# Optimization experiments

Measured on AMD Instinct MI355X. Metric: run time of the kernel, lower is better.

The kernel has to match this reference:

```python
import jax, jax.numpy as jnp
import numpy as np

NEG_SLOPE = 0.2   # PyG GATConv default negative_slope
LN_EPS = 1e-5

B, N, D, HID, HEADS = 4, 10000, 128, 256, 2
F_HEAD = HID // HEADS  # 128
E_RAND = 160000


def setup_inputs() -> dict:
    key = jax.random.key(0)
    ks = jax.random.split(key, 12)
    src = jax.random.randint(ks[0], (E_RAND,), 0, N, dtype=jnp.int32)
    dst = jax.random.randint(ks[1], (E_RAND,), 0, N, dtype=jnp.int32)
    loops = jnp.arange(N, dtype=jnp.int32)  # PyG GATConv adds self-loops
    edge_index = jnp.stack([jnp.concatenate([src, loops]),
                            jnp.concatenate([dst, loops])])  # [2, 170000]
    feature = jax.random.normal(ks[2], (B, N, D), jnp.float32)

    def w(k, shape):
        return jax.random.normal(k, shape, jnp.float32) * 0.05

    return {
        "feature": feature,
        "edge_index": edge_index,
        # layer 1: in D=128 -> heads*F_HEAD = 256
        "W1": w(ks[3], (D, HEADS * F_HEAD)),
        "a_src1": w(ks[4], (HEADS, F_HEAD)),
        "a_dst1": w(ks[5], (HEADS, F_HEAD)),
        "b1": jnp.zeros((HEADS * F_HEAD,), jnp.float32),
        "g1": jnp.ones((HID,), jnp.float32),
        "be1": jnp.zeros((HID,), jnp.float32),
        # layer 2: in 256 -> 256
        "W2": w(ks[6], (HID, HEADS * F_HEAD)),
        "a_src2": w(ks[7], (HEADS, F_HEAD)),
        "a_dst2": w(ks[8], (HEADS, F_HEAD)),
        "b2": jnp.zeros((HEADS * F_HEAD,), jnp.float32),
        "g2": jnp.ones((HID,), jnp.float32),
        "be2": jnp.zeros((HID,), jnp.float32),
    }


def _layer_norm(x, g, b):
    mu = jnp.mean(x, axis=-1, keepdims=True)
    var = jnp.mean(jnp.square(x - mu), axis=-1, keepdims=True)
    return (x - mu) * jax.lax.rsqrt(var + LN_EPS) * g + b


def _gat_conv(x, src, dst, W, a_src, a_dst, b):
    """PyG-style GATConv (concat=True), single graph. x: [N, Din]."""
    n = x.shape[0]
    h = (x @ W).reshape(n, HEADS, F_HEAD)              # [N,H,F]
    al_s = jnp.sum(h * a_src, axis=-1)                  # [N,H]
    al_d = jnp.sum(h * a_dst, axis=-1)                  # [N,H]
    e = jax.nn.leaky_relu(al_s[src] + al_d[dst], NEG_SLOPE)  # [E,H]
    # segment softmax over destination node (self-loops guarantee nonempty)
    m = jax.ops.segment_max(e, dst, num_segments=n)     # [N,H]
    ex = jnp.exp(e - m[dst])
    denom = jax.ops.segment_sum(ex, dst, num_segments=n)
    alpha = ex / (denom[dst] + 1e-16)                   # [E,H]
    msg = h[src] * alpha[..., None]                     # [E,H,F]
    out = jax.ops.segment_sum(msg, dst, num_segments=n) # [N,H,F]
    return out.reshape(n, HEADS * F_HEAD) + b


def reference(feature, edge_index, W1, a_src1, a_dst1, b1, g1, be1,
              W2, a_src2, a_dst2, b2, g2, be2):
    src, dst = edge_index[0], edge_index[1]

    def per_graph(x):
        h = _gat_conv(x, src, dst, W1, a_src1, a_dst1, b1)
        h = jax.nn.relu(_layer_norm(h, g1, be1))  # dropout off (eval)
        h = _gat_conv(h, src, dst, W2, a_src2, a_dst2, b2)
        h = jax.nn.relu(_layer_norm(h, g2, be2))
        return h

    return jax.vmap(per_graph)(feature)  # [B, N, HID]
```

## Files before the change

### kernel.cpp

```cpp
#include <hip/hip_runtime.h>
#include <hip/hip_bf16.h>

#define NN   10000
#define BB   4
#define DD   128
#define HIDD 256
#define NEG  0.2f

using bf16 = __hip_bfloat16;
typedef __bf16 bf16x8 __attribute__((ext_vector_type(8)));
typedef float  f32x4  __attribute__((ext_vector_type(4)));

__device__ __forceinline__ float lrelu(float x) { return x > 0.f ? x : NEG * x; }

__device__ __forceinline__ unsigned pack2(float a, float b) {
    unsigned lo = __bfloat16_as_ushort(__float2bfloat16(a));
    unsigned hi = __bfloat16_as_ushort(__float2bfloat16(b));
    return lo | (hi << 16);
}

__global__ void convert_kernel(const float* __restrict__ x, bf16* __restrict__ y, int n) {
    int i = blockIdx.x * 256 + threadIdx.x;
    if (i < n) y[i] = __float2bfloat16(x[i]);
}

__global__ void prep_kernel(int* counts,
                            const float* __restrict__ W1, bf16* __restrict__ Wt1,
                            const float* __restrict__ W2, bf16* __restrict__ Wt2) {
    int idx = blockIdx.x * 256 + threadIdx.x;
    if (idx < NN) { counts[idx] = 0; return; }
    idx -= NN;
    if (idx < DD * HIDD) {
        int k = idx / HIDD, n = idx % HIDD;
        Wt1[(size_t)n * DD + k] = __float2bfloat16(W1[idx]);
        return;
    }
    idx -= DD * HIDD;
    if (idx < HIDD * HIDD) {
        int k = idx / HIDD, n = idx % HIDD;
        Wt2[(size_t)n * HIDD + k] = __float2bfloat16(W2[idx]);
    }
}

__global__ void hist_kernel(const int* __restrict__ dstv, int* counts, int E) {
    int e = blockIdx.x * 256 + threadIdx.x;
    if (e < E) atomicAdd(&counts[dstv[e]], 1);
}

__global__ __launch_bounds__(1024) void scan_kernel(const int* __restrict__ counts,
                                                    int* row_start, int* cursor) {
    __shared__ int part[1024];
    int t = threadIdx.x;
    const int CH = (NN + 1023) / 1024;
    int base = t * CH;
    int s = 0;
    for (int j = 0; j < CH; j++) { int idx = base + j; if (idx < NN) s += counts[idx]; }
    part[t] = s;
    __syncthreads();
    for (int off = 1; off < 1024; off <<= 1) {
        int v = (t >= off) ? part[t - off] : 0;
        __syncthreads();
        part[t] += v;
        __syncthreads();
    }
    int excl = (t == 0) ? 0 : part[t - 1];
    for (int j = 0; j < CH; j++) {
        int idx = base + j;
        if (idx < NN) { row_start[idx] = excl; cursor[idx] = excl; excl += counts[idx]; }
    }
    if (t == 1023) row_start[NN] = part[1023];
}

__global__ void scatter_kernel(const int* __restrict__ srcv, const int* __restrict__ dstv,
                               int* cursor, int* csr_src, int E) {
    int e = blockIdx.x * 256 + threadIdx.x;
    if (e < E) {
        int d = dstv[e];
        int p = atomicAdd(&cursor[d], 1);
        csr_src[p] = srcv[e];
    }
}

template <int K>
__global__ __launch_bounds__(256) void gemm_kernel(const bf16* __restrict__ A,
                                                   const bf16* __restrict__ Wt,
                                                   const float* __restrict__ a_src,
                                                   const float* __restrict__ a_dst,
                                                   bf16* __restrict__ H,
                                                   float* __restrict__ als,
                                                   float* __restrict__ ald) {
    constexpr int NF = K / 32;
    __shared__ bf16 Bs[8 * NF * 512];

    int b     = blockIdx.x;
    int g     = b & 3;
    int r     = b >> 2;
    int head  = r & 1;
    int split = r >> 1;
    int wave  = threadIdx.x >> 6, lane = threadIdx.x & 63;
    int lm    = lane & 15, lq = lane >> 4;

    const bf16* Wh = Wt + (size_t)head * 128 * K;

#pragma unroll
    for (int jj = 0; jj < 2 * NF; jj++) {
        int j  = wave * 2 * NF + jj;
        int fi = j / NF, ks = j % NF;
        const bf16* src = Wh + (size_t)(fi * 16 + lm) * K + ks * 32 + lq * 8;
        __builtin_amdgcn_global_load_lds(
            (const __attribute__((address_space(1))) void*)src,
            (__attribute__((address_space(3))) void*)(Bs + j * 512),
            16, 0, 0);
    }
    __syncthreads();

    float4 asv[8], adv[8];
#pragma unroll
    for (int fi = 0; fi < 8; fi++) {
        asv[fi] = *(const float4*)(a_src + head * 128 + fi * 16 + lq * 4);
        adv[fi] = *(const float4*)(a_dst + head * 128 + fi * 16 + lq * 4);
    }

    const int NT = (NN + 127) / 128;
    for (int tt = split; tt < NT; tt += 64) {
        int m0 = tt * 128 + wave * 32;
        int rA = min(m0 + lm, NN - 1);
        int rB = min(m0 + 16 + lm, NN - 1);
        const bf16* Ar0 = A + ((size_t)g * NN + rA) * K + lq * 8;
        const bf16* Ar1 = A + ((size_t)g * NN + rB) * K + lq * 8;

        bf16x8 a0[NF], a1[NF];
#pragma unroll
        for (int ks = 0; ks < NF; ks++) {
            a0[ks] = *(const bf16x8*)(Ar0 + ks * 32);
            a1[ks] = *(const bf16x8*)(Ar1 + ks * 32);
        }

        f32x4 acc[2][8];
#pragma unroll
        for (int rb = 0; rb < 2; rb++)
#pragma unroll
            for (int i = 0; i < 8; i++) acc[rb][i] = (f32x4){0.f, 0.f, 0.f, 0.f};

#pragma unroll
        for (int ks = 0; ks < NF; ks++) {
#pragma unroll
            for (int fi = 0; fi < 8; fi++) {
                bf16x8 bv = *(const bf16x8*)(Bs + ((size_t)(fi * NF + ks) * 64 + lane) * 8);
                acc[0][fi] = __builtin_amdgcn_mfma_f32_16x16x32_bf16(bv, a0[ks], acc[0][fi], 0, 0, 0);
                acc[1][fi] = __builtin_amdgcn_mfma_f32_16x16x32_bf16(bv, a1[ks], acc[1][fi], 0, 0, 0);
            }
        }

#pragma unroll
        for (int rb = 0; rb < 2; rb++) {
            int nd = m0 + rb * 16 + lm;
            float ps = 0.f, pd = 0.f;
            bool ok = nd < NN;
            size_t hb = ((size_t)g * NN + (ok ? nd : 0)) * HIDD + head * 128 + lq * 4;
#pragma unroll
            for (int fi = 0; fi < 8; fi++) {
                f32x4 v = acc[rb][fi];
                ps += v[0] * asv[fi].x + v[1] * asv[fi].y + v[2] * asv[fi].z + v[3] * asv[fi].w;
                pd += v[0] * adv[fi].x + v[1] * adv[fi].y + v[2] * adv[fi].z + v[3] * adv[fi].w;
                if (ok) {
                    uint2 pk = {pack2(v[0], v[1]), pack2(v[2], v[3])};
                    *(uint2*)(H + hb + fi * 16) = pk;
                }
            }
            ps += __shfl_xor(ps, 16); ps += __shfl_xor(ps, 32);
            pd += __shfl_xor(pd, 16); pd += __shfl_xor(pd, 32);
            if (lq == 0 && ok) {
                als[((size_t)g * NN + nd) * 2 + head] = ps;
                ald[((size_t)g * NN + nd) * 2 + head] = pd;
            }
        }
    }
}

template <typename OT>
__global__ __launch_bounds__(256) void node_kernel(const int* __restrict__ row_start,
                                                   const int* __restrict__ csr_src,
                                                   const float2* __restrict__ als2,
                                                   const float2* __restrict__ ald2,
                                                   const bf16* __restrict__ H,
                                                   const float* __restrict__ bias,
                                                   const float* __restrict__ gam,
                                                   const float* __restrict__ bet,
                                                   OT* __restrict__ out) {
    int b = blockIdx.x;
    int g = b & 3;
    int wave = threadIdx.x >> 6, lane = threadIdx.x & 63;
    int n = (b >> 2) * 4 + wave;
    if (n >= NN) return;
    int start = row_start[n];
    int deg   = row_start[n + 1] - start;

    int grp = lane >> 5, lch = lane & 31;
    int hd_g = lch >> 4;
    const float* alsf = (const float*)(als2 + (size_t)g * NN);
    float2 ad = ald2[(size_t)g * NN + n];
    float adh = hd_g ? ad.y : ad.x;
    const int* Sr = csr_src + start;
    const bf16* Hg = H + (size_t)g * NN * HIDD;

    float acc[8] = {0.f, 0.f, 0.f, 0.f, 0.f, 0.f, 0.f, 0.f};
    float dsum = 0.f;

#define EDGE_FMA(ss, qq)                                                \
    {                                                                   \
        float wv = __expf(lrelu(alsf[(size_t)(ss) * 2 + hd_g] + adh));  \
        dsum += wv;                                                     \
        acc[0] = fmaf(wv, __uint_as_float(qq.x << 16), acc[0]);         \
        acc[1] = fmaf(wv, __uint_as_float(qq.x & 0xffff0000u), acc[1]); \
        acc[2] = fmaf(wv, __uint_as_float(qq.y << 16), acc[2]);         \
        acc[3] = fmaf(wv, __uint_as_float(qq.y & 0xffff0000u), acc[3]); \
        acc[4] = fmaf(wv, __uint_as_float(qq.z << 16), acc[4]);         \
        acc[5] = fmaf(wv, __uint_as_float(qq.z & 0xffff0000u), acc[5]); \
        acc[6] = fmaf(wv, __uint_as_float(qq.w << 16), acc[6]);         \
        acc[7] = fmaf(wv, __uint_as_float(qq.w & 0xffff0000u), acc[7]); \
    }

    int i = grp;
    for (; i + 6 < deg; i += 8) {
        int s0 = Sr[i], s1 = Sr[i + 2], s2 = Sr[i + 4], s3 = Sr[i + 6];
        uint4 q0 = *(const uint4*)(Hg + (size_t)s0 * HIDD + lch * 8);
        uint4 q1 = *(const uint4*)(Hg + (size_t)s1 * HIDD + lch * 8);
        uint4 q2 = *(const uint4*)(Hg + (size_t)s2 * HIDD + lch * 8);
        uint4 q3 = *(const uint4*)(Hg + (size_t)s3 * HIDD + lch * 8);
        EDGE_FMA(s0, q0)
        EDGE_FMA(s1, q1)
        EDGE_FMA(s2, q2)
        EDGE_FMA(s3, q3)
    }
    for (; i < deg; i += 2) {
        int s0 = Sr[i];
        uint4 q0 = *(const uint4*)(Hg + (size_t)s0 * HIDD + lch * 8);
        EDGE_FMA(s0, q0)
    }
#undef EDGE_FMA

#pragma unroll
    for (int j = 0; j < 8; j++) acc[j] += __shfl_xor(acc[j], 32);
    dsum += __shfl_xor(dsum, 32);
    float rdh = 1.f / dsum;

    float4 bi0 = *(const float4*)(bias + lch * 8);
    float4 bi1 = *(const float4*)(bias + lch * 8 + 4);
    float v[8];
    v[0] = fmaf(acc[0], rdh, bi0.x); v[1] = fmaf(acc[1], rdh, bi0.y);
    v[2] = fmaf(acc[2], rdh, bi0.z); v[3] = fmaf(acc[3], rdh, bi0.w);
    v[4] = fmaf(acc[4], rdh, bi1.x); v[5] = fmaf(acc[5], rdh, bi1.y);
    v[6] = fmaf(acc[6], rdh, bi1.z); v[7] = fmaf(acc[7], rdh, bi1.w);

    float s1 = 0.f, s2 = 0.f;
#pragma unroll
    for (int j = 0; j < 8; j++) { s1 += v[j]; s2 += v[j] * v[j]; }
#pragma unroll
    for (int off = 16; off; off >>= 1) {
        s1 += __shfl_xor(s1, off);
        s2 += __shfl_xor(s2, off);
    }
    float mu  = s1 * (1.f / HIDD);
    float var = s2 * (1.f / HIDD) - mu * mu;
    float rs  = rsqrtf(var + 1e-5f);

    float4 ga0 = *(const float4*)(gam + lch * 8);
    float4 ga1 = *(const float4*)(gam + lch * 8 + 4);
    float4 be0 = *(const float4*)(bet + lch * 8);
    float4 be1 = *(const float4*)(bet + lch * 8 + 4);
    float gaf[8] = {ga0.x, ga0.y, ga0.z, ga0.w, ga1.x, ga1.y, ga1.z, ga1.w};
    float bef[8] = {be0.x, be0.y, be0.z, be0.w, be1.x, be1.y, be1.z, be1.w};

    float o[8];
#pragma unroll
    for (int j = 0; j < 8; j++)
        o[j] = fmaxf((v[j] - mu) * rs * gaf[j] + bef[j], 0.f);

    if (grp == 0) {
        size_t base = ((size_t)g * NN + n) * HIDD + lch * 8;
        if constexpr (sizeof(OT) == 2) {
            uint4 pk;
            pk.x = pack2(o[0], o[1]); pk.y = pack2(o[2], o[3]);
            pk.z = pack2(o[4], o[5]); pk.w = pack2(o[6], o[7]);
            *(uint4*)((bf16*)out + base) = pk;
        } else {
            *(float4*)((float*)out + base)     = make_float4(o[0], o[1], o[2], o[3]);
            *(float4*)((float*)out + base + 4) = make_float4(o[4], o[5], o[6], o[7]);
        }
    }
}

extern "C" void kernel_launch(void* const* d_in, const int* in_sizes, int n_in,
                              void* d_out, int out_size, void* d_ws, size_t ws_size,
                              hipStream_t stream) {
    const float* feature = (const float*)d_in[0];
    const int*   ei      = (const int*)d_in[1];
    const float* W1      = (const float*)d_in[2];
    const float* a_src1  = (const float*)d_in[3];
    const float* a_dst1  = (const float*)d_in[4];
    const float* b1      = (const float*)d_in[5];
    const float* g1      = (const float*)d_in[6];
    const float* be1     = (const float*)d_in[7];
    const float* W2      = (const float*)d_in[8];
    const float* a_src2  = (const float*)d_in[9];
    const float* a_dst2  = (const float*)d_in[10];
    const float* b2      = (const float*)d_in[11];
    const float* g2      = (const float*)d_in[12];
    const float* be2     = (const float*)d_in[13];
    float* out = (float*)d_out;

    const int E = in_sizes[1] / 2;
    const int* srcv = ei;
    const int* dstv = ei + E;

    char* w = (char*)d_ws;
    auto alloc = [&](size_t bytes) -> char* {
        char* p = w;
        w += (bytes + 255) & ~(size_t)255;
        return p;
    };
    int*    counts    = (int*)alloc(sizeof(int) * NN);
    int*    row_start = (int*)alloc(sizeof(int) * (NN + 1));
    int*    cursor    = (int*)alloc(sizeof(int) * NN);
    int*    csr_src   = (int*)alloc(sizeof(int) * E);
    float*  als       = (float*)alloc(sizeof(float) * (size_t)BB * NN * 2);
    float*  ald       = (float*)alloc(sizeof(float) * (size_t)BB * NN * 2);
    bf16*   featbf    = (bf16*)alloc(sizeof(bf16) * (size_t)BB * NN * DD);
    bf16*   h         = (bf16*)alloc(sizeof(bf16) * (size_t)BB * NN * HIDD);
    bf16*   x2        = (bf16*)alloc(sizeof(bf16) * (size_t)BB * NN * HIDD);
    bf16*   Wt1       = (bf16*)alloc(sizeof(bf16) * DD * HIDD);
    bf16*   Wt2       = (bf16*)alloc(sizeof(bf16) * HIDD * HIDD);

    int nblk = ((NN + 3) / 4) * 4;
    int gblk = 4 * 2 * 64;

    {
        int ptot = NN + DD * HIDD + HIDD * HIDD;
        prep_kernel<<<(ptot + 255) / 256, 256, 0, stream>>>(counts, W1, Wt1, W2, Wt2);
        int nf = BB * NN * DD;
        convert_kernel<<<(nf + 255) / 256, 256, 0, stream>>>(feature, featbf, nf);
    }
    hist_kernel<<<(E + 255) / 256, 256, 0, stream>>>(dstv, counts, E);
    scan_kernel<<<1, 1024, 0, stream>>>(counts, row_start, cursor);
    scatter_kernel<<<(E + 255) / 256, 256, 0, stream>>>(srcv, dstv, cursor, csr_src, E);

    gemm_kernel<DD><<<gblk, 256, 0, stream>>>(featbf, Wt1, a_src1, a_dst1, h, als, ald);
    node_kernel<bf16><<<nblk, 256, 0, stream>>>(row_start, csr_src, (const float2*)als, (const float2*)ald,
                                                h, b1, g1, be1, x2);

    gemm_kernel<HIDD><<<gblk, 256, 0, stream>>>(x2, Wt2, a_src2, a_dst2, h, als, ald);
    node_kernel<float><<<nblk, 256, 0, stream>>>(row_start, csr_src, (const float2*)als, (const float2*)ald,
                                                 h, b2, g2, be2, out);
}
```

Measured before the change: 264.1 us.

## Use one 256-row tile per 512-thread GEMM block and deepen edge unroll

Result: slower. 285.4 us (+8.1%).

```diff
diff --git a/kernel.cpp b/kernel.cpp
--- a/kernel.cpp
+++ b/kernel.cpp
@@ -82,7 +82,7 @@
 }
 
 template <int K>
-__global__ __launch_bounds__(256) void gemm_kernel(const bf16* __restrict__ A,
+__global__ __launch_bounds__(512) void gemm_kernel(const bf16* __restrict__ A,
                                                    const bf16* __restrict__ Wt,
                                                    const float* __restrict__ a_src,
                                                    const float* __restrict__ a_dst,
@@ -96,20 +96,18 @@
     int g     = b & 3;
     int r     = b >> 2;
     int head  = r & 1;
-    int split = r >> 1;
+    int tile  = r >> 1;
     int wave  = threadIdx.x >> 6, lane = threadIdx.x & 63;
     int lm    = lane & 15, lq = lane >> 4;
 
     const bf16* Wh = Wt + (size_t)head * 128 * K;
 
 #pragma unroll
-    for (int jj = 0; jj < 2 * NF; jj++) {
-        int j  = wave * 2 * NF + jj;
-        int fi = j / NF, ks = j % NF;
-        const bf16* src = Wh + (size_t)(fi * 16 + lm) * K + ks * 32 + lq * 8;
+    for (int ks = 0; ks < NF; ks++) {
+        const bf16* src = Wh + (size_t)(wave * 16 + lm) * K + ks * 32 + lq * 8;
         __builtin_amdgcn_global_load_lds(
             (const __attribute__((address_space(1))) void*)src,
-            (__attribute__((address_space(3))) void*)(Bs + j * 512),
+            (__attribute__((address_space(3))) void*)(Bs + (wave * NF + ks) * 512),
             16, 0, 0);
     }
     __syncthreads();
@@ -121,59 +119,51 @@
         adv[fi] = *(const float4*)(a_dst + head * 128 + fi * 16 + lq * 4);
     }
 
-    const int NT = (NN + 127) / 128;
-    for (int tt = split; tt < NT; tt += 64) {
-        int m0 = tt * 128 + wave * 32;
-        int rA = min(m0 + lm, NN - 1);
-        int rB = min(m0 + 16 + lm, NN - 1);
-        const bf16* Ar0 = A + ((size_t)g * NN + rA) * K + lq * 8;
-        const bf16* Ar1 = A + ((size_t)g * NN + rB) * K + lq * 8;
-
-        bf16x8 a0[NF], a1[NF];
-#pragma unroll
-        for (int ks = 0; ks < NF; ks++) {
-            a0[ks] = *(const bf16x8*)(Ar0 + ks * 32);
-            a1[ks] = *(const bf16x8*)(Ar1 + ks * 32);
+    int m0 = tile * 256 + wave * 32;
+    int rA = min(m0 + lm, NN - 1);
+    int rB = min(m0 + 16 + lm, NN - 1);
+    const bf16* Ar0 = A + ((size_t)g * NN + rA) * K + lq * 8;
+    const bf16* Ar1 = A + ((size_t)g * NN + rB) * K + lq * 8;
+
+    f32x4 acc[2][8];
+#pragma unroll
+    for (int rb = 0; rb < 2; rb++)
+#pragma unroll
+        for (int i = 0; i < 8; i++) acc[rb][i] = (f32x4){0.f, 0.f, 0.f, 0.f};
+
+#pragma unroll
+    for (int ks = 0; ks < NF; ks++) {
+        bf16x8 a0 = *(const bf16x8*)(Ar0 + ks * 32);
+        bf16x8 a1 = *(const bf16x8*)(Ar1 + ks * 32);
+#pragma unroll
+        for (int fi = 0; fi < 8; fi++) {
+            bf16x8 bv = *(const bf16x8*)(Bs + ((size_t)(fi * NF + ks) * 64 + lane) * 8);
+            acc[0][fi] = __builtin_amdgcn_mfma_f32_16x16x32_bf16(bv, a0, acc[0][fi], 0, 0, 0);
+            acc[1][fi] = __builtin_amdgcn_mfma_f32_16x16x32_bf16(bv, a1, acc[1][fi], 0, 0, 0);
         }
-
-        f32x4 acc[2][8];
-#pragma unroll
-        for (int rb = 0; rb < 2; rb++)
-#pragma unroll
-            for (int i = 0; i < 8; i++) acc[rb][i] = (f32x4){0.f, 0.f, 0.f, 0.f};
-
-#pragma unroll
-        for (int ks = 0; ks < NF; ks++) {
-#pragma unroll
-            for (int fi = 0; fi < 8; fi++) {
-                bf16x8 bv = *(const bf16x8*)(Bs + ((size_t)(fi * NF + ks) * 64 + lane) * 8);
-                acc[0][fi] = __builtin_amdgcn_mfma_f32_16x16x32_bf16(bv, a0[ks], acc[0][fi], 0, 0, 0);
-                acc[1][fi] = __builtin_amdgcn_mfma_f32_16x16x32_bf16(bv, a1[ks], acc[1][fi], 0, 0, 0);
+    }
+
+#pragma unroll
+    for (int rb = 0; rb < 2; rb++) {
+        int nd = m0 + rb * 16 + lm;
+        float ps = 0.f, pd = 0.f;
+        bool ok = nd < NN;
+        size_t hb = ((size_t)g * NN + (ok ? nd : 0)) * HIDD + head * 128 + lq * 4;
+#pragma unroll
+        for (int fi = 0; fi < 8; fi++) {
+            f32x4 v = acc[rb][fi];
+            ps += v[0] * asv[fi].x + v[1] * asv[fi].y + v[2] * asv[fi].z + v[3] * asv[fi].w;
+            pd += v[0] * adv[fi].x + v[1] * adv[fi].y + v[2] * adv[fi].z + v[3] * adv[fi].w;
+            if (ok) {
+                uint2 pk = {pack2(v[0], v[1]), pack2(v[2], v[3])};
+                *(uint2*)(H + hb + fi * 16) = pk;
             }
         }
-
-#pragma unroll
-        for (int rb = 0; rb < 2; rb++) {
-            int nd = m0 + rb * 16 + lm;
-            float ps = 0.f, pd = 0.f;
-            bool ok = nd < NN;
-            size_t hb = ((size_t)g * NN + (ok ? nd : 0)) * HIDD + head * 128 + lq * 4;
-#pragma unroll
-            for (int fi = 0; fi < 8; fi++) {
-                f32x4 v = acc[rb][fi];
-                ps += v[0] * asv[fi].x + v[1] * asv[fi].y + v[2] * asv[fi].z + v[3] * asv[fi].w;
-                pd += v[0] * adv[fi].x + v[1] * adv[fi].y + v[2] * adv[fi].z + v[3] * adv[fi].w;
-                if (ok) {
-                    uint2 pk = {pack2(v[0], v[1]), pack2(v[2], v[3])};
-                    *(uint2*)(H + hb + fi * 16) = pk;
-                }
-            }
-            ps += __shfl_xor(ps, 16); ps += __shfl_xor(ps, 32);
-            pd += __shfl_xor(pd, 16); pd += __shfl_xor(pd, 32);
-            if (lq == 0 && ok) {
-                als[((size_t)g * NN + nd) * 2 + head] = ps;
-                ald[((size_t)g * NN + nd) * 2 + head] = pd;
-            }
+        ps += __shfl_xor(ps, 16); ps += __shfl_xor(ps, 32);
+        pd += __shfl_xor(pd, 16); pd += __shfl_xor(pd, 32);
+        if (lq == 0 && ok) {
+            als[((size_t)g * NN + nd) * 2 + head] = ps;
+            ald[((size_t)g * NN + nd) * 2 + head] = pd;
         }
     }
 }
@@ -222,6 +212,26 @@
     }
 
     int i = grp;
+    for (; i + 14 < deg; i += 16) {
+        int s0 = Sr[i],      s1 = Sr[i + 2],  s2 = Sr[i + 4],  s3 = Sr[i + 6];
+        int s4 = Sr[i + 8],  s5 = Sr[i + 10], s6 = Sr[i + 12], s7 = Sr[i + 14];
+        uint4 q0 = *(const uint4*)(Hg + (size_t)s0 * HIDD + lch * 8);
+        uint4 q1 = *(const uint4*)(Hg + (size_t)s1 * HIDD + lch * 8);
+        uint4 q2 = *(const uint4*)(Hg + (size_t)s2 * HIDD + lch * 8);
+        uint4 q3 = *(const uint4*)(Hg + (size_t)s3 * HIDD + lch * 8);
+        uint4 q4 = *(const uint4*)(Hg + (size_t)s4 * HIDD + lch * 8);
+        uint4 q5 = *(const uint4*)(Hg + (size_t)s5 * HIDD + lch * 8);
+        uint4 q6 = *(const uint4*)(Hg + (size_t)s6 * HIDD + lch * 8);
+        uint4 q7 = *(const uint4*)(Hg + (size_t)s7 * HIDD + lch * 8);
+        EDGE_FMA(s0, q0)
+        EDGE_FMA(s1, q1)
+        EDGE_FMA(s2, q2)
+        EDGE_FMA(s3, q3)
+        EDGE_FMA(s4, q4)
+        EDGE_FMA(s5, q5)
+        EDGE_FMA(s6, q6)
+        EDGE_FMA(s7, q7)
+    }
     for (; i + 6 < deg; i += 8) {
         int s0 = Sr[i], s1 = Sr[i + 2], s2 = Sr[i + 4], s3 = Sr[i + 6];
         uint4 q0 = *(const uint4*)(Hg + (size_t)s0 * HIDD + lch * 8);
@@ -333,7 +343,7 @@
     bf16*   Wt2       = (bf16*)alloc(sizeof(bf16) * HIDD * HIDD);
 
     int nblk = ((NN + 3) / 4) * 4;
-    int gblk = 4 * 2 * 64;
+    int gblk = 4 * 2 * ((NN + 255) / 256);
 
     {
         int ptot = NN + DD * HIDD + HIDD * HIDD;
@@ -345,11 +355,11 @@
     scan_kernel<<<1, 1024, 0, stream>>>(counts, row_start, cursor);
     scatter_kernel<<<(E + 255) / 256, 256, 0, stream>>>(srcv, dstv, cursor, csr_src, E);
 
-    gemm_kernel<DD><<<gblk, 256, 0, stream>>>(featbf, Wt1, a_src1, a_dst1, h, als, ald);
+    gemm_kernel<DD><<<gblk, 512, 0, stream>>>(featbf, Wt1, a_src1, a_dst1, h, als, ald);
     node_kernel<bf16><<<nblk, 256, 0, stream>>>(row_start, csr_src, (const float2*)als, (const float2*)ald,
                                                 h, b1, g1, be1, x2);
 
-    gemm_kernel<HIDD><<<gblk, 256, 0, stream>>>(x2, Wt2, a_src2, a_dst2, h, als, ald);
+    gemm_kernel<HIDD><<<gblk, 512, 0, stream>>>(x2, Wt2, a_src2, a_dst2, h, als, ald);
     node_kernel<float><<<nblk, 256, 0, stream>>>(row_start, csr_src, (const float2*)als, (const float2*)ald,
                                                  h, b2, g2, be2, out);
 }
```

## Restructure GEMM to one tile per block with K-chunked LDS and fuse feature convert

Applied to the files above, without the earlier changes.

Measured after the change: 252.1 us. 1.05x faster.

```diff
diff --git a/kernel.cpp b/kernel.cpp
--- a/kernel.cpp
+++ b/kernel.cpp
@@ -19,15 +19,19 @@
     return lo | (hi << 16);
 }
 
-__global__ void convert_kernel(const float* __restrict__ x, bf16* __restrict__ y, int n) {
-    int i = blockIdx.x * 256 + threadIdx.x;
-    if (i < n) y[i] = __float2bfloat16(x[i]);
-}
-
-__global__ void prep_kernel(int* counts,
+#define NF4 (BB * NN * DD / 4)
+__global__ void prep_kernel(const float* __restrict__ feat, bf16* __restrict__ featbf,
+                            int* counts,
                             const float* __restrict__ W1, bf16* __restrict__ Wt1,
                             const float* __restrict__ W2, bf16* __restrict__ Wt2) {
     int idx = blockIdx.x * 256 + threadIdx.x;
+    if (idx < NF4) {
+        float4 v = *(const float4*)(feat + (size_t)idx * 4);
+        uint2 pk = {pack2(v.x, v.y), pack2(v.z, v.w)};
+        *(uint2*)(featbf + (size_t)idx * 4) = pk;
+        return;
+    }
+    idx -= NF4;
     if (idx < NN) { counts[idx] = 0; return; }
     idx -= NN;
     if (idx < DD * HIDD) {
@@ -89,30 +93,59 @@
                                                    bf16* __restrict__ H,
                                                    float* __restrict__ als,
                                                    float* __restrict__ ald) {
-    constexpr int NF = K / 32;
-    __shared__ bf16 Bs[8 * NF * 512];
-
-    int b     = blockIdx.x;
-    int g     = b & 3;
-    int r     = b >> 2;
-    int head  = r & 1;
-    int split = r >> 1;
-    int wave  = threadIdx.x >> 6, lane = threadIdx.x & 63;
-    int lm    = lane & 15, lq = lane >> 4;
-
-    const bf16* Wh = Wt + (size_t)head * 128 * K;
-
-#pragma unroll
-    for (int jj = 0; jj < 2 * NF; jj++) {
-        int j  = wave * 2 * NF + jj;
-        int fi = j / NF, ks = j % NF;
-        const bf16* src = Wh + (size_t)(fi * 16 + lm) * K + ks * 32 + lq * 8;
-        __builtin_amdgcn_global_load_lds(
-            (const __attribute__((address_space(1))) void*)src,
-            (__attribute__((address_space(3))) void*)(Bs + j * 512),
-            16, 0, 0);
-    }
-    __syncthreads();
+    __shared__ bf16 Bs[128 * 128];
+
+    int b    = blockIdx.x;
+    int g    = b & 3;
+    int r    = b >> 2;
+    int head = r & 1;
+    int wave = threadIdx.x >> 6;
+    int m0   = (r >> 1) * 128 + wave * 32;
+    int lane = threadIdx.x & 63;
+    int lm   = lane & 15, lq = lane >> 4;
+
+    int rowA = min(m0 + lm, NN - 1);
+    int rowB = min(m0 + 16 + lm, NN - 1);
+    const bf16* Ar0 = A + ((size_t)g * NN + rowA) * K + lq * 8;
+    const bf16* Ar1 = A + ((size_t)g * NN + rowB) * K + lq * 8;
+    const bf16* Wh  = Wt + (size_t)head * 128 * K;
+
+    f32x4 acc[2][8];
+#pragma unroll
+    for (int rb = 0; rb < 2; rb++)
+#pragma unroll
+        for (int i = 0; i < 8; i++) acc[rb][i] = (f32x4){0.f, 0.f, 0.f, 0.f};
+
+    for (int kb = 0; kb < K; kb += 128) {
+        if (kb) __syncthreads();
+#pragma unroll
+        for (int jj = 0; jj < 8; jj++) {
+            int j  = wave * 8 + jj;
+            int fi = j >> 2, ks = j & 3;
+            const bf16* src = Wh + (size_t)(fi * 16 + lm) * K + kb + ks * 32 + lq * 8;
+            __builtin_amdgcn_global_load_lds(
+                (const __attribute__((address_space(1))) void*)src,
+                (__attribute__((address_space(3))) void*)(Bs + j * 512),
+                16, 0, 0);
+        }
+        __syncthreads();
+
+        bf16x8 a0[4], a1[4];
+#pragma unroll
+        for (int ks = 0; ks < 4; ks++) {
+            a0[ks] = *(const bf16x8*)(Ar0 + kb + ks * 32);
+            a1[ks] = *(const bf16x8*)(Ar1 + kb + ks * 32);
+        }
+#pragma unroll
+        for (int ks = 0; ks < 4; ks++) {
+#pragma unroll
+            for (int fi = 0; fi < 8; fi++) {
+                bf16x8 bv = *(const bf16x8*)(Bs + ((fi * 4 + ks) * 64 + lane) * 8);
+                acc[0][fi] = __builtin_amdgcn_mfma_f32_16x16x32_bf16(bv, a0[ks], acc[0][fi], 0, 0, 0);
+                acc[1][fi] = __builtin_amdgcn_mfma_f32_16x16x32_bf16(bv, a1[ks], acc[1][fi], 0, 0, 0);
+            }
+        }
+    }
 
     float4 asv[8], adv[8];
 #pragma unroll
@@ -121,59 +154,27 @@
         adv[fi] = *(const float4*)(a_dst + head * 128 + fi * 16 + lq * 4);
     }
 
-    const int NT = (NN + 127) / 128;
-    for (int tt = split; tt < NT; tt += 64) {
-        int m0 = tt * 128 + wave * 32;
-        int rA = min(m0 + lm, NN - 1);
-        int rB = min(m0 + 16 + lm, NN - 1);
-        const bf16* Ar0 = A + ((size_t)g * NN + rA) * K + lq * 8;
-        const bf16* Ar1 = A + ((size_t)g * NN + rB) * K + lq * 8;
-
-        bf16x8 a0[NF], a1[NF];
-#pragma unroll
-        for (int ks = 0; ks < NF; ks++) {
-            a0[ks] = *(const bf16x8*)(Ar0 + ks * 32);
-            a1[ks] = *(const bf16x8*)(Ar1 + ks * 32);
-        }
-
-        f32x4 acc[2][8];
-#pragma unroll
-        for (int rb = 0; rb < 2; rb++)
-#pragma unroll
-            for (int i = 0; i < 8; i++) acc[rb][i] = (f32x4){0.f, 0.f, 0.f, 0.f};
-
-#pragma unroll
-        for (int ks = 0; ks < NF; ks++) {
-#pragma unroll
-            for (int fi = 0; fi < 8; fi++) {
-                bf16x8 bv = *(const bf16x8*)(Bs + ((size_t)(fi * NF + ks) * 64 + lane) * 8);
-                acc[0][fi] = __builtin_amdgcn_mfma_f32_16x16x32_bf16(bv, a0[ks], acc[0][fi], 0, 0, 0);
-                acc[1][fi] = __builtin_amdgcn_mfma_f32_16x16x32_bf16(bv, a1[ks], acc[1][fi], 0, 0, 0);
+#pragma unroll
+    for (int rb = 0; rb < 2; rb++) {
+        int nd = m0 + rb * 16 + lm;
+        float ps = 0.f, pd = 0.f;
+        bool ok = nd < NN;
+        size_t hb = ((size_t)g * NN + (ok ? nd : 0)) * HIDD + head * 128 + lq * 4;
+#pragma unroll
+        for (int fi = 0; fi < 8; fi++) {
+            f32x4 v = acc[rb][fi];
+            ps += v[0] * asv[fi].x + v[1] * asv[fi].y + v[2] * asv[fi].z + v[3] * asv[fi].w;
+            pd += v[0] * adv[fi].x + v[1] * adv[fi].y + v[2] * adv[fi].z + v[3] * adv[fi].w;
+            if (ok) {
+                uint2 pk = {pack2(v[0], v[1]), pack2(v[2], v[3])};
+                *(uint2*)(H + hb + fi * 16) = pk;
             }
         }
-
-#pragma unroll
-        for (int rb = 0; rb < 2; rb++) {
-            int nd = m0 + rb * 16 + lm;
-            float ps = 0.f, pd = 0.f;
-            bool ok = nd < NN;
-            size_t hb = ((size_t)g * NN + (ok ? nd : 0)) * HIDD + head * 128 + lq * 4;
-#pragma unroll
-            for (int fi = 0; fi < 8; fi++) {
-                f32x4 v = acc[rb][fi];
-                ps += v[0] * asv[fi].x + v[1] * asv[fi].y + v[2] * asv[fi].z + v[3] * asv[fi].w;
-                pd += v[0] * adv[fi].x + v[1] * adv[fi].y + v[2] * adv[fi].z + v[3] * adv[fi].w;
-                if (ok) {
-                    uint2 pk = {pack2(v[0], v[1]), pack2(v[2], v[3])};
-                    *(uint2*)(H + hb + fi * 16) = pk;
-                }
-            }
-            ps += __shfl_xor(ps, 16); ps += __shfl_xor(ps, 32);
-            pd += __shfl_xor(pd, 16); pd += __shfl_xor(pd, 32);
-            if (lq == 0 && ok) {
-                als[((size_t)g * NN + nd) * 2 + head] = ps;
-                ald[((size_t)g * NN + nd) * 2 + head] = pd;
-            }
+        ps += __shfl_xor(ps, 16); ps += __shfl_xor(ps, 32);
+        pd += __shfl_xor(pd, 16); pd += __shfl_xor(pd, 32);
+        if (lq == 0 && ok) {
+            als[((size_t)g * NN + nd) * 2 + head] = ps;
+            ald[((size_t)g * NN + nd) * 2 + head] = pd;
         }
     }
 }
@@ -333,13 +334,11 @@
     bf16*   Wt2       = (bf16*)alloc(sizeof(bf16) * HIDD * HIDD);
 
     int nblk = ((NN + 3) / 4) * 4;
-    int gblk = 4 * 2 * 64;
+    int gblk = 4 * 2 * ((NN + 127) / 128);
 
     {
-        int ptot = NN + DD * HIDD + HIDD * HIDD;
-        prep_kernel<<<(ptot + 255) / 256, 256, 0, stream>>>(counts, W1, Wt1, W2, Wt2);
-        int nf = BB * NN * DD;
-        convert_kernel<<<(nf + 255) / 256, 256, 0, stream>>>(feature, featbf, nf);
+        int ptot = NF4 + NN + DD * HIDD + HIDD * HIDD;
+        prep_kernel<<<(ptot + 255) / 256, 256, 0, stream>>>(feature, featbf, counts, W1, Wt1, W2, Wt2);
     }
     hist_kernel<<<(E + 255) / 256, 256, 0, stream>>>(dstv, counts, E);
     scan_kernel<<<1, 1024, 0, stream>>>(counts, row_start, cursor);
```
